# Optimization experiments

Measured on AMD Instinct MI355X. Metric: run time of the kernel, lower is better.

The kernel has to match this reference:

```python
import jax, jax.numpy as jnp
import numpy as np

B, E, S, DIM, HID, H = 8, 512, 1024, 1024, 1024, 8  # S == DIM == HID by construction


def setup_inputs() -> dict:
    key = jax.random.key(0)
    ks = jax.random.split(key, 7)
    x = jax.random.normal(ks[0], (B, E, S), dtype=jnp.float32)
    # per-head projection Linear(dim, hidden_dim): weight [H, hidden, dim], bias [H, hidden]
    proj_w = jax.random.normal(ks[1], (H, HID, DIM), dtype=jnp.float32) / np.sqrt(DIM)
    proj_b = jax.random.normal(ks[2], (H, HID), dtype=jnp.float32) * 0.02
    # per-head ColRepeatCausalLinear: weight [H, S] (torch.randn(1, dim)), bias [H, S] (zeros init)
    mix_w = jax.random.normal(ks[3], (H, S), dtype=jnp.float32)
    mix_b = jnp.zeros((H, S), dtype=jnp.float32)
    # out_proj Linear(dim, dim)
    out_w = jax.random.normal(ks[4], (DIM, DIM), dtype=jnp.float32) / np.sqrt(DIM)
    out_b = jax.random.normal(ks[5], (DIM,), dtype=jnp.float32) * 0.02
    return {"x": x, "proj_w": proj_w, "proj_b": proj_b, "mix_w": mix_w,
            "mix_b": mix_b, "out_w": out_w, "out_b": out_b, "index": 0}


def reference(x, proj_w, proj_b, mix_w, mix_b, out_w, out_b, index):
    # Per-head linear projection on the last axis (grouped GEMM across heads).
    # proj: [B, H, E, HID]
    proj = jnp.einsum('bes,hds->bhed', x, proj_w) + proj_b[None, :, None, :]
    # ColRepeatCausalLinear parallel path with decay_value == 1:
    # W[i, j] = v[j] for j >= i  =>  (x @ W)[..., j] = v[j] * cumsum(x, -1)[..., j]
    mixed = mix_w[None, :, None, :] * jnp.cumsum(proj, axis=-1) + mix_b[None, :, None, :]
    # torch.cat(activations, dim=1): [B, H*E, S]
    hidden = mixed.reshape(B, H * E, S)
    # out_proj Linear(dim, dim) on last axis
    out = hidden @ out_w.T + out_b
    return out
```

## Files before the change

### kernel.cpp

```cpp
#include <hip/hip_runtime.h>

#define NH    8
#define NE    512
#define NB    8
#define ND    1024
#define NROW  4096

typedef unsigned short u16;
typedef __attribute__((ext_vector_type(8))) short short8;
typedef __attribute__((ext_vector_type(4))) float f32x4;

__device__ __forceinline__ u16 f2bf(float f) {
  unsigned int u = __float_as_uint(f);
  u += 0x7fffu + ((u >> 16) & 1u);
  return (u16)(u >> 16);
}

__device__ __forceinline__ void gload16(const u16* g, u16* l) {
  __builtin_amdgcn_global_load_lds(
      (const __attribute__((address_space(1))) unsigned int*)(const void*)g,
      (__attribute__((address_space(3))) unsigned int*)(void*)l, 16, 0, 0);
}

__global__ __launch_bounds__(256) void convert_x_kernel(const float* __restrict__ X,
                                                        u16* __restrict__ Xb) {
  int i = blockIdx.x * 256 + threadIdx.x;
  float4 v = ((const float4*)X)[i];
  ushort4 o;
  o.x = f2bf(v.x); o.y = f2bf(v.y); o.z = f2bf(v.z); o.w = f2bf(v.w);
  ((ushort4*)Xb)[i] = o;
}

__global__ __launch_bounds__(256) void transpose_w_kernel(const float* __restrict__ W,
                                                          u16* __restrict__ Wt) {
  __shared__ float tile[64][65];
  int h  = blockIdx.z;
  int s0 = blockIdx.x * 64;
  int d0 = blockIdx.y * 64;
  int t  = threadIdx.x;
  int tr = t >> 4;
  int tc = t & 15;
#pragma unroll
  for (int i = 0; i < 4; ++i) {
    int d = tr + i * 16;
    float4 v = *(const float4*)(W + ((size_t)h * ND + d0 + d) * ND + s0 + tc * 4);
    tile[d][tc * 4 + 0] = v.x;
    tile[d][tc * 4 + 1] = v.y;
    tile[d][tc * 4 + 2] = v.z;
    tile[d][tc * 4 + 3] = v.w;
  }
  __syncthreads();
#pragma unroll
  for (int i = 0; i < 4; ++i) {
    int s  = tr + i * 16;
    int dd = tc * 4;
    ushort4 o;
    o.x = f2bf(tile[dd + 0][s]);
    o.y = f2bf(tile[dd + 1][s]);
    o.z = f2bf(tile[dd + 2][s]);
    o.w = f2bf(tile[dd + 3][s]);
    *(ushort4*)(Wt + ((size_t)h * ND + s0 + s) * ND + d0 + dd) = o;
  }
}

__global__ __launch_bounds__(256) void scan_kernel(const float* __restrict__ out_w,
                                                   const float* __restrict__ mix_w,
                                                   const float* __restrict__ mix_b,
                                                   const float* __restrict__ proj_b,
                                                   const float* __restrict__ out_b,
                                                   u16* __restrict__ Afac,
                                                   float* __restrict__ Kc) {
  int h = blockIdx.x >> 10;
  int o = blockIdx.x & 1023;
  int t = threadIdx.x;
  int lane = t & 63, wave = t >> 6;
  const float* owr = out_w + (size_t)o * ND;
  const float* mwr = mix_w + (size_t)h * ND;
  const float* mbr = mix_b + (size_t)h * ND;
  const float* pbr = proj_b + (size_t)h * ND;

  float l[4];
  float run = 0.f, mbdot = 0.f;
#pragma unroll
  for (int k = 0; k < 4; ++k) {
    int j = 1023 - (4 * t + k);
    float ow = owr[j];
    mbdot += ow * mbr[j];
    run += ow * mwr[j];
    l[k] = run;
  }
  float tsum = run;
  float sc = tsum;
#pragma unroll
  for (int d = 1; d < 64; d <<= 1) {
    float other = __shfl_up(sc, d);
    if (lane >= d) sc += other;
  }
  __shared__ float wsum[4];
  __shared__ float red[4];
  if (lane == 63) wsum[wave] = sc;
  __syncthreads();
  float wprefix = 0.f;
  for (int w = 0; w < wave; ++w) wprefix += wsum[w];
  float excl = wprefix + sc - tsum;

  float cdot = 0.f;
  ushort4 pack;
  u16* pk = (u16*)&pack;
#pragma unroll
  for (int k = 0; k < 4; ++k) {
    int d = 1023 - (4 * t + k);
    float a = excl + l[k];
    cdot += a * pbr[d];
    pk[3 - k] = f2bf(a);
  }
  *(ushort4*)(Afac + ((size_t)(h * ND + o)) * ND + (1020 - 4 * t)) = pack;

  float tot = cdot + mbdot;
#pragma unroll
  for (int m = 32; m >= 1; m >>= 1) tot += __shfl_xor(tot, m);
  if (lane == 0) red[wave] = tot;
  __syncthreads();
  if (t == 0) {
    Kc[h * ND + o] = red[0] + red[1] + red[2] + red[3] + out_b[o];
  }
}

#define MFMA_(d, a, b) d = __builtin_amdgcn_mfma_f32_16x16x32_bf16(a, b, d, 0, 0, 0)
#define NOVM ((void)0)
#define VM6 asm volatile("s_waitcnt vmcnt(6)" ::: "memory")
#define VM0 asm volatile("s_waitcnt vmcnt(0)" ::: "memory")

#define PHASE(q, b, STAGE_STMT, VMSTMT) do {                                   \
    short8 a00 = ldA(b, 2*(q),     0);                                         \
    short8 a01 = ldA(b, 2*(q),     1);                                         \
    short8 a10 = ldA(b, 2*(q) + 1, 0);                                         \
    short8 a11 = ldA(b, 2*(q) + 1, 1);                                         \
    if ((q) == 0) {                                                            \
      bf00 = ldB(b, 0, 0); bf01 = ldB(b, 0, 1);                                \
      bf10 = ldB(b, 1, 0); bf11 = ldB(b, 1, 1);                                \
      bf20 = ldB(b, 2, 0); bf21 = ldB(b, 2, 1);                                \
      bf30 = ldB(b, 3, 0); bf31 = ldB(b, 3, 1);                                \
    }                                                                          \
    STAGE_STMT;                                                                \
    __builtin_amdgcn_sched_barrier(0);                                         \
    VMSTMT;                                                                    \
    __builtin_amdgcn_s_barrier();                                              \
    asm volatile("s_waitcnt lgkmcnt(0)" ::: "memory");                         \
    __builtin_amdgcn_sched_barrier(0);                                         \
    __builtin_amdgcn_s_setprio(1);                                             \
    MFMA_(acc[2*(q)  ][0], a00, bf00);                                         \
    MFMA_(acc[2*(q)  ][1], a00, bf10);                                         \
    MFMA_(acc[2*(q)  ][2], a00, bf20);                                         \
    MFMA_(acc[2*(q)  ][3], a00, bf30);                                         \
    MFMA_(acc[2*(q)+1][0], a10, bf00);                                         \
    MFMA_(acc[2*(q)+1][1], a10, bf10);                                         \
    MFMA_(acc[2*(q)+1][2], a10, bf20);                                         \
    MFMA_(acc[2*(q)+1][3], a10, bf30);                                         \
    MFMA_(acc[2*(q)  ][0], a01, bf01);                                         \
    MFMA_(acc[2*(q)  ][1], a01, bf11);                                         \
    MFMA_(acc[2*(q)  ][2], a01, bf21);                                         \
    MFMA_(acc[2*(q)  ][3], a01, bf31);                                         \
    MFMA_(acc[2*(q)+1][0], a11, bf01);                                         \
    MFMA_(acc[2*(q)+1][1], a11, bf11);                                         \
    MFMA_(acc[2*(q)+1][2], a11, bf21);                                         \
    MFMA_(acc[2*(q)+1][3], a11, bf31);                                         \
    __builtin_amdgcn_s_setprio(0);                                             \
    __builtin_amdgcn_s_barrier();                                              \
  } while (0)

#define GEMM_8PH_BODY(ASRC, BSRC)                                              \
  const int tid  = threadIdx.x;                                                \
  const int lane = tid & 63;                                                   \
  const int wave = tid >> 6;                                                   \
  const int wm   = wave >> 2;                                                  \
  const int wn   = wave & 3;                                                   \
  const int li8 = lane >> 3;                                                   \
  const int lc  = (lane & 7) ^ li8;                                            \
  const size_t stSrc = (size_t)li8 * ND + lc * 8;                              \
  const int stDst = lane * 8;                                                  \
  const u16* aSrc = (ASRC) + stSrc;                                            \
  const u16* bSrc = (BSRC) + stSrc;                                            \
  const int fr  = lane & 15;                                                   \
  const int rg  = lane >> 4;                                                   \
  const int ca0 = (((lane >> 4)    ) ^ (lane & 7)) * 8;                        \
  const int ca1 = (((lane >> 4) + 4) ^ (lane & 7)) * 8;                        \
  const int aOff = (wm * 128 + fr) * 64;                                       \
  const int bOff = 16384 + (wn * 64 + fr) * 64;                                \
  auto stageA = [&](int h, int t, int b) {                                     \
    _Pragma("unroll")                                                          \
    for (int jj = 0; jj < 2; ++jj) {                                           \
      int j = 2 * wave + jj;                                                   \
      int R = ((j >> 3) << 7) + h * 64 + ((j & 7) << 3);                       \
      gload16(aSrc + (size_t)R * ND + t * 64, lds + b * 32768 + R * 64 + stDst); \
    }                                                                          \
  };                                                                           \
  auto stageB = [&](int h, int t, int b) {                                     \
    _Pragma("unroll")                                                          \
    for (int jj = 0; jj < 2; ++jj) {                                           \
      int j = 2 * wave + jj;                                                   \
      int R = h * 128 + j * 8;                                                 \
      gload16(bSrc + (size_t)R * ND + t * 64, lds + b * 32768 + 16384 + R * 64 + stDst); \
    }                                                                          \
  };                                                                           \
  auto ldA = [&](int b, int mi, int kk) -> short8 {                            \
    return *(const short8*)(lds + b * 32768 + aOff + mi * 1024 + (kk ? ca1 : ca0)); \
  };                                                                           \
  auto ldB = [&](int b, int ni, int kk) -> short8 {                            \
    return *(const short8*)(lds + b * 32768 + bOff + ni * 1024 + (kk ? ca1 : ca0)); \
  };                                                                           \
  f32x4 acc[8][4];                                                             \
  f32x4 z = {0.f, 0.f, 0.f, 0.f};                                              \
  _Pragma("unroll")                                                            \
  for (int i = 0; i < 8; ++i)                                                  \
    _Pragma("unroll")                                                          \
    for (int j = 0; j < 4; ++j) acc[i][j] = z;                                 \
  short8 bf00, bf01, bf10, bf11, bf20, bf21, bf30, bf31;                       \
  stageA(0, 0, 0); stageA(1, 0, 0);                                            \
  stageB(0, 0, 0); stageB(1, 0, 0);                                            \
  stageB(0, 1, 1); stageB(1, 1, 1);                                            \
  stageA(0, 1, 1);                                                             \
  asm volatile("s_waitcnt vmcnt(6)" ::: "memory");                             \
  __builtin_amdgcn_s_barrier();                                                \
  _Pragma("unroll 1")                                                          \
  for (int it = 0; it < 7; ++it) {                                             \
    const int T = 2 * it;                                                      \
    PHASE(0, 0, stageA(1, T + 1, 1), NOVM);                                    \
    PHASE(1, 0, stageB(0, T + 2, 0), NOVM);                                    \
    PHASE(2, 0, stageB(1, T + 2, 0), NOVM);                                    \
    PHASE(3, 0, stageA(0, T + 2, 0), VM6);                                     \
    PHASE(0, 1, stageA(1, T + 2, 0), NOVM);                                    \
    PHASE(1, 1, stageB(0, T + 3, 1), NOVM);                                    \
    PHASE(2, 1, stageB(1, T + 3, 1), NOVM);                                    \
    PHASE(3, 1, stageA(0, T + 3, 1), VM6);                                     \
  }                                                                            \
  PHASE(0, 0, stageA(1, 15, 1), NOVM);                                         \
  PHASE(1, 0, NOVM, NOVM);                                                     \
  PHASE(2, 0, NOVM, NOVM);                                                     \
  PHASE(3, 0, NOVM, VM0);                                                      \
  PHASE(0, 1, NOVM, NOVM);                                                     \
  PHASE(1, 1, NOVM, NOVM);                                                     \
  PHASE(2, 1, NOVM, NOVM);                                                     \
  PHASE(3, 1, NOVM, NOVM);

__global__ __launch_bounds__(512, 2) void gemm1_8ph(const u16* __restrict__ Afac,
                                                    const u16* __restrict__ Wt,
                                                    u16* __restrict__ Mmat) {
  __shared__ __align__(16) u16 lds[65536];
  const int h  = blockIdx.z;
  const int m0 = blockIdx.y * 256;
  const int n0 = blockIdx.x * 256;
  GEMM_8PH_BODY(Afac + ((size_t)h * ND + m0) * ND, Wt + ((size_t)h * ND + n0) * ND)

  u16* Mh = Mmat + (size_t)h * ND * ND;
  const int r0 = m0 + wm * 128 + rg * 4;
  const int c0 = n0 + wn * 64 + fr;
#pragma unroll
  for (int mi = 0; mi < 8; ++mi) {
#pragma unroll
    for (int r = 0; r < 4; ++r) {
      u16* orow = Mh + (size_t)(r0 + mi * 16 + r) * ND + c0;
#pragma unroll
      for (int ni = 0; ni < 4; ++ni)
        orow[ni * 16] = f2bf(acc[mi][ni][r]);
    }
  }
}

__global__ __launch_bounds__(512, 2) void gemm2_8ph(const u16* __restrict__ Xb,
                                                    const u16* __restrict__ Bm,
                                                    const float* __restrict__ Kc,
                                                    float* __restrict__ Out) {
  __shared__ __align__(16) u16 lds[65536];
  const int bid = blockIdx.x;
  const int swz = (bid & 7) * 64 + (bid >> 3);
  const int m0  = (swz >> 5) * 256;
  const int n0  = (swz & 31) * 256;
  GEMM_8PH_BODY(Xb + (size_t)m0 * ND, Bm + (size_t)n0 * ND)

  const int hH = n0 >> 10;
  const int r0 = m0 + wm * 128 + rg * 4;
  const int c0 = n0 + wn * 64 + fr;
  const int o0 = c0 & 1023;
  float bias[4];
#pragma unroll
  for (int ni = 0; ni < 4; ++ni) bias[ni] = Kc[c0 + ni * 16];
#pragma unroll
  for (int mi = 0; mi < 8; ++mi) {
#pragma unroll
    for (int r = 0; r < 4; ++r) {
      int rb = r0 + mi * 16 + r;
      float* orow = Out + ((size_t)(rb >> 9) * 4096 + hH * 512 + (rb & 511)) * 1024 + o0;
#pragma unroll
      for (int ni = 0; ni < 4; ++ni)
        orow[ni * 16] = acc[mi][ni][r] + bias[ni];
    }
  }
}

extern "C" void kernel_launch(void* const* d_in, const int* in_sizes, int n_in,
                              void* d_out, int out_size, void* d_ws, size_t ws_size,
                              hipStream_t stream) {
  (void)in_sizes; (void)n_in; (void)out_size; (void)ws_size;
  const float* x      = (const float*)d_in[0];
  const float* proj_w = (const float*)d_in[1];
  const float* proj_b = (const float*)d_in[2];
  const float* mix_w  = (const float*)d_in[3];
  const float* mix_b  = (const float*)d_in[4];
  const float* out_w  = (const float*)d_in[5];
  const float* out_b  = (const float*)d_in[6];
  float* Out = (float*)d_out;

  u16* Wt   = (u16*)d_out;
  u16* Afac = (u16*)d_out + (size_t)8 * 1024 * 1024;
  u16*   Xb   = (u16*)d_ws;
  u16*   Mmat = (u16*)((char*)d_ws + ((size_t)8 << 20));
  float* Kc   = (float*)((char*)d_ws + ((size_t)24 << 20));

  convert_x_kernel<<<4096, 256, 0, stream>>>(x, Xb);
  transpose_w_kernel<<<dim3(16, 16, NH), 256, 0, stream>>>(proj_w, Wt);
  scan_kernel<<<NH * ND, 256, 0, stream>>>(out_w, mix_w, mix_b, proj_b, out_b, Afac, Kc);
  gemm1_8ph<<<dim3(4, 4, NH), 512, 0, stream>>>(Afac, Wt, Mmat);
  gemm2_8ph<<<512, 512, 0, stream>>>(Xb, Mmat, Kc, Out);
}
```

Baseline: 131.8 us.

## Halve gemm1 M-tile to 128 rows and loop heads inside scan kernel

```diff
diff --git a/kernel.cpp b/kernel.cpp
--- a/kernel.cpp
+++ b/kernel.cpp
@@ -63,72 +63,77 @@
   }
 }
 
-__global__ __launch_bounds__(256) void scan_kernel(const float* __restrict__ out_w,
-                                                   const float* __restrict__ mix_w,
-                                                   const float* __restrict__ mix_b,
-                                                   const float* __restrict__ proj_b,
-                                                   const float* __restrict__ out_b,
-                                                   u16* __restrict__ Afac,
-                                                   float* __restrict__ Kc) {
-  int h = blockIdx.x >> 10;
-  int o = blockIdx.x & 1023;
+__global__ __launch_bounds__(256) void scan2_kernel(const float* __restrict__ out_w,
+                                                    const float* __restrict__ mix_w,
+                                                    const float* __restrict__ mix_b,
+                                                    const float* __restrict__ proj_b,
+                                                    const float* __restrict__ out_b,
+                                                    u16* __restrict__ Afac,
+                                                    float* __restrict__ Kc) {
+  int o = blockIdx.x;
   int t = threadIdx.x;
   int lane = t & 63, wave = t >> 6;
-  const float* owr = out_w + (size_t)o * ND;
-  const float* mwr = mix_w + (size_t)h * ND;
-  const float* mbr = mix_b + (size_t)h * ND;
-  const float* pbr = proj_b + (size_t)h * ND;
-
-  float l[4];
-  float run = 0.f, mbdot = 0.f;
-#pragma unroll
-  for (int k = 0; k < 4; ++k) {
-    int j = 1023 - (4 * t + k);
-    float ow = owr[j];
-    mbdot += ow * mbr[j];
-    run += ow * mwr[j];
-    l[k] = run;
-  }
-  float tsum = run;
-  float sc = tsum;
-#pragma unroll
-  for (int d = 1; d < 64; d <<= 1) {
-    float other = __shfl_up(sc, d);
-    if (lane >= d) sc += other;
-  }
   __shared__ float wsum[4];
   __shared__ float red[4];
-  if (lane == 63) wsum[wave] = sc;
-  __syncthreads();
-  float wprefix = 0.f;
-  for (int w = 0; w < wave; ++w) wprefix += wsum[w];
-  float excl = wprefix + sc - tsum;
-
-  float cdot = 0.f;
-  ushort4 pack;
-  u16* pk = (u16*)&pack;
-#pragma unroll
-  for (int k = 0; k < 4; ++k) {
-    int d = 1023 - (4 * t + k);
-    float a = excl + l[k];
-    cdot += a * pbr[d];
-    pk[3 - k] = f2bf(a);
-  }
-  *(ushort4*)(Afac + ((size_t)(h * ND + o)) * ND + (1020 - 4 * t)) = pack;
-
-  float tot = cdot + mbdot;
-#pragma unroll
-  for (int m = 32; m >= 1; m >>= 1) tot += __shfl_xor(tot, m);
-  if (lane == 0) red[wave] = tot;
-  __syncthreads();
-  if (t == 0) {
-    Kc[h * ND + o] = red[0] + red[1] + red[2] + red[3] + out_b[o];
+
+  float ow[4];
+#pragma unroll
+  for (int k = 0; k < 4; ++k) ow[k] = out_w[(size_t)o * ND + 1023 - (4 * t + k)];
+  float ob = out_b[o];
+
+#pragma unroll 1
+  for (int h = 0; h < NH; ++h) {
+    const float* mwr = mix_w + (size_t)h * ND;
+    const float* mbr = mix_b + (size_t)h * ND;
+    const float* pbr = proj_b + (size_t)h * ND;
+
+    float l[4];
+    float run = 0.f, mbdot = 0.f;
+#pragma unroll
+    for (int k = 0; k < 4; ++k) {
+      int j = 1023 - (4 * t + k);
+      mbdot += ow[k] * mbr[j];
+      run += ow[k] * mwr[j];
+      l[k] = run;
+    }
+    float tsum = run;
+    float sc = tsum;
+#pragma unroll
+    for (int d = 1; d < 64; d <<= 1) {
+      float other = __shfl_up(sc, d);
+      if (lane >= d) sc += other;
+    }
+    if (lane == 63) wsum[wave] = sc;
+    __syncthreads();
+    float wprefix = 0.f;
+    for (int w = 0; w < wave; ++w) wprefix += wsum[w];
+    float excl = wprefix + sc - tsum;
+
+    float cdot = 0.f;
+    ushort4 pack;
+    u16* pk = (u16*)&pack;
+#pragma unroll
+    for (int k = 0; k < 4; ++k) {
+      int d = 1023 - (4 * t + k);
+      float a = excl + l[k];
+      cdot += a * pbr[d];
+      pk[3 - k] = f2bf(a);
+    }
+    *(ushort4*)(Afac + ((size_t)(h * ND + o)) * ND + (1020 - 4 * t)) = pack;
+
+    float tot = cdot + mbdot;
+#pragma unroll
+    for (int m = 32; m >= 1; m >>= 1) tot += __shfl_xor(tot, m);
+    if (lane == 0) red[wave] = tot;
+    __syncthreads();
+    if (t == 0) Kc[h * ND + o] = red[0] + red[1] + red[2] + red[3] + ob;
   }
 }
 
 #define MFMA_(d, a, b) d = __builtin_amdgcn_mfma_f32_16x16x32_bf16(a, b, d, 0, 0, 0)
 #define NOVM ((void)0)
 #define VM6 asm volatile("s_waitcnt vmcnt(6)" ::: "memory")
+#define VM5 asm volatile("s_waitcnt vmcnt(5)" ::: "memory")
 #define VM0 asm volatile("s_waitcnt vmcnt(0)" ::: "memory")
 
 #define PHASE(q, b, STAGE_STMT, VMSTMT) do {                                   \
@@ -165,6 +170,34 @@
     MFMA_(acc[2*(q)+1][1], a11, bf11);                                         \
     MFMA_(acc[2*(q)+1][2], a11, bf21);                                         \
     MFMA_(acc[2*(q)+1][3], a11, bf31);                                         \
+    __builtin_amdgcn_s_setprio(0);                                             \
+    __builtin_amdgcn_s_barrier();                                              \
+  } while (0)
+
+#define PHASE1(q, b, STAGE_STMT, VMSTMT) do {                                  \
+    short8 a0 = ldA(b, (q), 0);                                                \
+    short8 a1 = ldA(b, (q), 1);                                                \
+    if ((q) == 0) {                                                            \
+      bf00 = ldB(b, 0, 0); bf01 = ldB(b, 0, 1);                                \
+      bf10 = ldB(b, 1, 0); bf11 = ldB(b, 1, 1);                                \
+      bf20 = ldB(b, 2, 0); bf21 = ldB(b, 2, 1);                                \
+      bf30 = ldB(b, 3, 0); bf31 = ldB(b, 3, 1);                                \
+    }                                                                          \
+    STAGE_STMT;                                                                \
+    __builtin_amdgcn_sched_barrier(0);                                         \
+    VMSTMT;                                                                    \
+    __builtin_amdgcn_s_barrier();                                              \
+    asm volatile("s_waitcnt lgkmcnt(0)" ::: "memory");                         \
+    __builtin_amdgcn_sched_barrier(0);                                         \
+    __builtin_amdgcn_s_setprio(1);                                             \
+    MFMA_(acc[(q)][0], a0, bf00);                                              \
+    MFMA_(acc[(q)][1], a0, bf10);                                              \
+    MFMA_(acc[(q)][2], a0, bf20);                                              \
+    MFMA_(acc[(q)][3], a0, bf30);                                              \
+    MFMA_(acc[(q)][0], a1, bf01);                                              \
+    MFMA_(acc[(q)][1], a1, bf11);                                              \
+    MFMA_(acc[(q)][2], a1, bf21);                                              \
+    MFMA_(acc[(q)][3], a1, bf31);                                              \
     __builtin_amdgcn_s_setprio(0);                                             \
     __builtin_amdgcn_s_barrier();                                              \
   } while (0)
@@ -246,17 +279,88 @@
 __global__ __launch_bounds__(512, 2) void gemm1_8ph(const u16* __restrict__ Afac,
                                                     const u16* __restrict__ Wt,
                                                     u16* __restrict__ Mmat) {
-  __shared__ __align__(16) u16 lds[65536];
+  __shared__ __align__(16) u16 lds[49152];
   const int h  = blockIdx.z;
-  const int m0 = blockIdx.y * 256;
+  const int m0 = blockIdx.y * 128;
   const int n0 = blockIdx.x * 256;
-  GEMM_8PH_BODY(Afac + ((size_t)h * ND + m0) * ND, Wt + ((size_t)h * ND + n0) * ND)
+  const int tid  = threadIdx.x;
+  const int lane = tid & 63;
+  const int wave = tid >> 6;
+  const int wm   = wave >> 2;
+  const int wn   = wave & 3;
+  const int li8 = lane >> 3;
+  const int lc  = (lane & 7) ^ li8;
+  const size_t stSrc = (size_t)li8 * ND + lc * 8;
+  const int stDst = lane * 8;
+  const u16* aSrc = Afac + ((size_t)h * ND + m0) * ND + stSrc;
+  const u16* bSrc = Wt + ((size_t)h * ND + n0) * ND + stSrc;
+  const int fr  = lane & 15;
+  const int rg  = lane >> 4;
+  const int ca0 = (((lane >> 4)    ) ^ (lane & 7)) * 8;
+  const int ca1 = (((lane >> 4) + 4) ^ (lane & 7)) * 8;
+  const int aOff = (wm * 64 + fr) * 64;
+  const int bOff = 8192 + (wn * 64 + fr) * 64;
+
+  auto stageA = [&](int h2, int t, int b) {
+    int R = (wave >> 2) * 64 + h2 * 32 + (wave & 3) * 8;
+    gload16(aSrc + (size_t)R * ND + t * 64, lds + b * 24576 + R * 64 + stDst);
+  };
+  auto stageB = [&](int h2, int t, int b) {
+#pragma unroll
+    for (int jj = 0; jj < 2; ++jj) {
+      int j = 2 * wave + jj;
+      int R = h2 * 128 + j * 8;
+      gload16(bSrc + (size_t)R * ND + t * 64, lds + b * 24576 + 8192 + R * 64 + stDst);
+    }
+  };
+  auto ldA = [&](int b, int mi, int kk) -> short8 {
+    return *(const short8*)(lds + b * 24576 + aOff + mi * 1024 + (kk ? ca1 : ca0));
+  };
+  auto ldB = [&](int b, int ni, int kk) -> short8 {
+    return *(const short8*)(lds + b * 24576 + bOff + ni * 1024 + (kk ? ca1 : ca0));
+  };
+
+  f32x4 acc[4][4];
+  f32x4 z = {0.f, 0.f, 0.f, 0.f};
+#pragma unroll
+  for (int i = 0; i < 4; ++i)
+#pragma unroll
+    for (int j = 0; j < 4; ++j) acc[i][j] = z;
+  short8 bf00, bf01, bf10, bf11, bf20, bf21, bf30, bf31;
+
+  stageA(0, 0, 0); stageA(1, 0, 0);
+  stageB(0, 0, 0); stageB(1, 0, 0);
+  stageB(0, 1, 1); stageB(1, 1, 1);
+  stageA(0, 1, 1);
+  VM5;
+  __builtin_amdgcn_s_barrier();
+
+#pragma unroll 1
+  for (int it = 0; it < 7; ++it) {
+    const int T = 2 * it;
+    PHASE1(0, 0, stageA(1, T + 1, 1), NOVM);
+    PHASE1(1, 0, stageB(0, T + 2, 0), NOVM);
+    PHASE1(2, 0, stageB(1, T + 2, 0), NOVM);
+    PHASE1(3, 0, stageA(0, T + 2, 0), VM5);
+    PHASE1(0, 1, stageA(1, T + 2, 0), NOVM);
+    PHASE1(1, 1, stageB(0, T + 3, 1), NOVM);
+    PHASE1(2, 1, stageB(1, T + 3, 1), NOVM);
+    PHASE1(3, 1, stageA(0, T + 3, 1), VM5);
+  }
+  PHASE1(0, 0, stageA(1, 15, 1), NOVM);
+  PHASE1(1, 0, NOVM, NOVM);
+  PHASE1(2, 0, NOVM, NOVM);
+  PHASE1(3, 0, NOVM, VM0);
+  PHASE1(0, 1, NOVM, NOVM);
+  PHASE1(1, 1, NOVM, NOVM);
+  PHASE1(2, 1, NOVM, NOVM);
+  PHASE1(3, 1, NOVM, NOVM);
 
   u16* Mh = Mmat + (size_t)h * ND * ND;
-  const int r0 = m0 + wm * 128 + rg * 4;
+  const int r0 = m0 + wm * 64 + rg * 4;
   const int c0 = n0 + wn * 64 + fr;
 #pragma unroll
-  for (int mi = 0; mi < 8; ++mi) {
+  for (int mi = 0; mi < 4; ++mi) {
 #pragma unroll
     for (int r = 0; r < 4; ++r) {
       u16* orow = Mh + (size_t)(r0 + mi * 16 + r) * ND + c0;
@@ -319,7 +423,7 @@
 
   convert_x_kernel<<<4096, 256, 0, stream>>>(x, Xb);
   transpose_w_kernel<<<dim3(16, 16, NH), 256, 0, stream>>>(proj_w, Wt);
-  scan_kernel<<<NH * ND, 256, 0, stream>>>(out_w, mix_w, mix_b, proj_b, out_b, Afac, Kc);
-  gemm1_8ph<<<dim3(4, 4, NH), 512, 0, stream>>>(Afac, Wt, Mmat);
+  scan2_kernel<<<ND, 256, 0, stream>>>(out_w, mix_w, mix_b, proj_b, out_b, Afac, Kc);
+  gemm1_8ph<<<dim3(4, 8, NH), 512, 0, stream>>>(Afac, Wt, Mmat);
   gemm2_8ph<<<512, 512, 0, stream>>>(Xb, Mmat, Kc, Out);
 }
```

Result: faster. 128.2 us (-2.8%).
